# Kernel optimization log

Measured on AMD Instinct MI355X. Metric: run time of the kernel, lower is better.

The kernel has to match this reference:

```python
import jax, jax.numpy as jnp
import numpy as np

TH_HIGH = 0.6
TH_LOW = 0.3
NEGPOS_RATIO = 3
VAR0, VAR1 = 0.1, 0.2
IMG_SIZE = 255.0


def point_form(a):
    # (cx,cy,w,h) -> (xmin,ymin,xmax,ymax)
    return jnp.concatenate([a[..., :2] - a[..., 2:] / 2,
                            a[..., :2] + a[..., 2:] / 2], axis=-1)


def jaccard(a, b):
    # a: [B,4] point form, b: [A,4] point form -> IoU [B,A]
    lt = jnp.maximum(a[:, None, :2], b[None, :, :2])
    rb = jnp.minimum(a[:, None, 2:], b[None, :, 2:])
    wh = jnp.clip(rb - lt, 0.0)
    inter = wh[..., 0] * wh[..., 1]
    area_a = ((a[:, 2] - a[:, 0]) * (a[:, 3] - a[:, 1]))[:, None]
    area_b = ((b[:, 2] - b[:, 0]) * (b[:, 3] - b[:, 1]))[None, :]
    return inter / (area_a + area_b - inter)


def encode(matched, priors):
    # matched: point form, priors: center-size form (standard SSD encode)
    g_cxcy = ((matched[..., :2] + matched[..., 2:]) / 2 - priors[..., :2]) / (VAR0 * priors[..., 2:])
    g_wh = jnp.log((matched[..., 2:] - matched[..., :2]) / priors[..., 2:]) / VAR1
    return jnp.concatenate([g_cxcy, g_wh], axis=-1)


def decode(loc, priors):
    # standard SSD decode -> point form boxes
    cxcy = priors[..., :2] + loc[..., :2] * VAR0 * priors[..., 2:]
    wh = priors[..., 2:] * jnp.exp(loc[..., 2:] * VAR1)
    mins = cxcy - wh / 2
    return jnp.concatenate([mins, mins + wh], axis=-1)


def smooth_l1(x):
    ax = jnp.abs(x)
    return jnp.where(ax < 1.0, 0.5 * x * x, ax - 0.5)


def setup_inputs() -> dict:
    key = jax.random.key(0)
    k1, k2, k3, k4 = jax.random.split(key, 4)
    B, G, S = 64, 128, 4
    A = G * G * S  # 65536 anchors
    c = (jnp.arange(G, dtype=jnp.float32) + 0.5) / G
    cxcy = jnp.stack(jnp.meshgrid(c, c, indexing='ij'), axis=-1).reshape(-1, 2)  # [G*G,2]
    scales = jnp.array([0.08, 0.12, 0.2, 0.3], dtype=jnp.float32)
    wh = jnp.stack([scales, scales], axis=-1)  # [S,2]
    anchors = jnp.concatenate([jnp.repeat(cxcy, S, axis=0), jnp.tile(wh, (G * G, 1))], axis=-1)  # [A,4] center-size
    # gt boxes: small jitter around a random anchor so positives exist
    idx = jax.random.randint(k1, (B,), 0, A)
    gt_cs = anchors[idx] * (1.0 + 0.03 * jax.random.normal(k2, (B, 4), dtype=jnp.float32))
    gt_boxes = point_form(gt_cs)  # [B,4] point form
    loc_pred = 0.5 * jax.random.normal(k3, (B, A, 4), dtype=jnp.float32)
    conf_pred = jax.random.normal(k4, (B, A, 2), dtype=jnp.float32)
    return {"loc_pred": loc_pred, "conf_pred": conf_pred, "gt_boxes": gt_boxes, "anchors": anchors}


def reference(loc_pred, conf_pred, gt_boxes, anchors):
    B, A, _ = loc_pred.shape
    pf_anchors = point_form(anchors)
    overlaps = jaccard(gt_boxes, pf_anchors)                      # [B,A]
    labels = (overlaps >= TH_HIGH).astype(jnp.int32) - \
             ((overlaps > TH_LOW) & (overlaps < TH_HIGH)).astype(jnp.int32)
    pos = labels == 1                                             # [B,A]
    neg0 = labels == 0
    N = pos.sum()
    Nf = jnp.maximum(N.astype(loc_pred.dtype), 1.0)

    loc_gt = encode(gt_boxes[:, None, :], anchors[None, :, :])    # [B,A,4]
    elem = smooth_l1(loc_pred - loc_gt)
    loss_loc = (elem * pos[..., None]).sum() / (Nf * 4.0)

    # --- hard negative mining ---
    logp = jax.nn.log_softmax(conf_pred, axis=-1)                 # [B,A,2]
    tgt = pos.astype(jnp.int32)
    nll = -jnp.take_along_axis(logp, tgt[..., None], axis=-1)[..., 0]  # [B,A]
    ce = jnp.where(neg0, nll, 0.0)
    loss_idx = jnp.argsort(-ce, axis=1)                           # descending
    idx_rank = jnp.argsort(loss_idx, axis=1)
    num_pos = pos.sum(axis=1, keepdims=True)
    num_neg = jnp.clip(NEGPOS_RATIO * num_pos, 10, A - 1)
    neg = idx_rank < num_neg                                      # [B,A]

    # --- weighted classification loss over picked pos+neg ---
    sel = pos | neg
    w = jnp.array([1.0 / 3.0, 1.0], dtype=conf_pred.dtype)
    wsel = jnp.where(sel, w[tgt], 0.0)
    loss_cls = (nll * wsel).sum() / wsel.sum()

    # --- accuracies on picked set ---
    pred_cls = jnp.argmax(conf_pred, axis=-1)
    pos_m = sel & (tgt == 1)
    neg_m = sel & (tgt == 0)
    pos_accuracy = ((pred_cls == 1) & pos_m).sum() / jnp.maximum(pos_m.sum(), 1)
    neg_accuracy = ((pred_cls == 0) & neg_m).sum() / jnp.maximum(neg_m.sum(), 1)

    # --- decoded diagnostics (masked means over positives) ---
    decoded = decode(loc_pred, anchors[None, :, :])               # [B,A,4] point form
    pos_err = jnp.linalg.norm((gt_boxes[:, None, :2] - decoded[..., :2]) * IMG_SIZE, axis=-1)
    position_error = (pos_err * pos).sum() / Nf
    size_diff = jnp.abs(gt_boxes[:, None, 2:] - decoded[..., 2:])  # [B,A,2]
    size_errors = (size_diff * pos[..., None]).sum(axis=(0, 1)) / Nf * IMG_SIZE

    return (loss_loc, loss_cls, pos_accuracy, neg_accuracy, position_error, size_errors, N)
```

## Files before the change

### kernel.cpp

```cpp
#include <hip/hip_runtime.h>
#include <math.h>


#define MAXB 64
#define BPR 16
#define APB 4096
#define KPT 16
#define NB2 4096
#define NB3 2048

struct Accum {
  int pnp[MAXB * BPR];
  int ppc[MAXB * BPR];
  float pf_loc[MAXB * BPR];
  float pf_clsp[MAXB * BPR];
  float pf_perr[MAXB * BPR];
  float pf_se0[MAXB * BPR];
  float pf_se1[MAXB * BPR];
  int cnum[MAXB];
  int b1[MAXB];
  int kr1[MAXB];
  float row_cls[MAXB];
  int row_ntot[MAXB];
  int row_ncor[MAXB];
};

__device__ __forceinline__ float iou_f(float4 g, float4 an) {
  float ax0 = an.x - an.z * 0.5f, ay0 = an.y - an.w * 0.5f;
  float ax1 = an.x + an.z * 0.5f, ay1 = an.y + an.w * 0.5f;
  float ltx = fmaxf(g.x, ax0), lty = fmaxf(g.y, ay0);
  float rbx = fminf(g.z, ax1), rby = fminf(g.w, ay1);
  float w = fmaxf(rbx - ltx, 0.f), h = fmaxf(rby - lty, 0.f);
  float inter = w * h;
  float area_g = (g.z - g.x) * (g.w - g.y);
  float area_a = (ax1 - ax0) * (ay1 - ay0);
  return inter / (area_g + area_a - inter);
}

__device__ __forceinline__ float sl1(float x) {
  float ax = fabsf(x);
  return ax < 1.f ? 0.5f * x * x : ax - 0.5f;
}

__device__ uint2 pick_l1(const unsigned int* __restrict__ g1, int b, int kr_in,
                         unsigned int* s_ws, volatile unsigned int* s_bin,
                         volatile unsigned int* s_kr) {
  int tid = threadIdx.x, lane = tid & 63, wv = tid >> 6;
  const unsigned int* base = g1 + b * BPR * 256;
  unsigned int my = 0;
#pragma unroll
  for (int s = 0; s < BPR; ++s) my += base[s * 256 + tid];
  unsigned int v = my;
#pragma unroll
  for (int o = 1; o < 64; o <<= 1) {
    unsigned int t = __shfl_down(v, o, 64);
    if (lane + o < 64) v += t;
  }
  if (lane == 0) s_ws[wv] = v;
  __syncthreads();
  unsigned int off = 0;
  for (int w2 = wv + 1; w2 < 4; ++w2) off += s_ws[w2];
  unsigned int incl = v + off, above = incl - my;
  if ((int)above < kr_in && kr_in <= (int)incl) {
    *s_bin = (unsigned int)tid;
    *s_kr = (unsigned int)(kr_in - (int)above);
  }
  __syncthreads();
  uint2 r;
  r.x = *s_bin;
  r.y = *s_kr;
  __syncthreads();
  return r;
}

template <int NB>
__device__ uint2 pick_hist(const unsigned int* __restrict__ h, int kr_in,
                           unsigned int* s_ws, volatile unsigned int* s_bin,
                           volatile unsigned int* s_kr) {
  int tid = threadIdx.x, lane = tid & 63, wv = tid >> 6;
  constexpr int PER = NB / 256;
  unsigned int loc[PER];
  unsigned int my = 0;
#pragma unroll
  for (int i = 0; i < PER; ++i) {
    loc[i] = h[tid * PER + i];
    my += loc[i];
  }
  unsigned int v = my;
#pragma unroll
  for (int o = 1; o < 64; o <<= 1) {
    unsigned int t = __shfl_down(v, o, 64);
    if (lane + o < 64) v += t;
  }
  if (lane == 0) s_ws[wv] = v;
  __syncthreads();
  unsigned int off = 0;
  for (int w2 = wv + 1; w2 < 4; ++w2) off += s_ws[w2];
  unsigned int incl = v + off, above = incl - my;
  if ((int)above < kr_in && kr_in <= (int)incl) {
    int kk = kr_in - (int)above;
#pragma unroll
    for (int i = PER - 1; i >= 0; --i) {
      int c = (int)loc[i];
      if (kk <= c) {
        *s_bin = (unsigned int)(tid * PER + i);
        *s_kr = (unsigned int)kk;
        break;
      }
      kk -= c;
    }
  }
  __syncthreads();
  uint2 r;
  r.x = *s_bin;
  r.y = *s_kr;
  __syncthreads();
  return r;
}

__global__ __launch_bounds__(256) void k_main(
    const float* __restrict__ loc_pred, const float* __restrict__ conf,
    const float* __restrict__ gt, const float* __restrict__ anchors,
    Accum* __restrict__ acc, unsigned int* __restrict__ g1,
    unsigned int* __restrict__ g2, int A) {
  int sl = blockIdx.x, b = blockIdx.y;
  int linear = b * BPR + sl;
  int tid = threadIdx.x, lane = tid & 63, wv = tid >> 6;
  __shared__ unsigned int hist[4][256];
  __shared__ float smf[5][4];
  __shared__ int smi[2][4];
  g2[linear * 256 + tid] = 0u;
  if (linear == 0 && tid < MAXB) acc->cnum[tid] = 0;
  for (int i = tid; i < 1024; i += 256) ((unsigned int*)hist)[i] = 0u;
  __syncthreads();

  float4 g4 = reinterpret_cast<const float4*>(gt)[b];
  const float4* conf4 = reinterpret_cast<const float4*>(conf);
  const float4* anc4 = reinterpret_cast<const float4*>(anchors);
  const float4* loc4 = reinterpret_cast<const float4*>(loc_pred);
  int abase = sl * APB;
  long long cbase = ((long long)b * A + abase) >> 1;

  float loc_s = 0.f, clsp = 0.f, perr = 0.f, se0 = 0.f, se1 = 0.f;
  int pcnt = 0, pcor = 0;

#pragma unroll
  for (int j = 0; j < 8; ++j) {
    float4 cc = conf4[cbase + tid + j * 256];
    int a0 = abase + 2 * (tid + j * 256);
#pragma unroll
    for (int h = 0; h < 2; ++h) {
      int a = a0 + h;
      float c0 = h ? cc.z : cc.x;
      float c1 = h ? cc.w : cc.y;
      float4 an = anc4[a];
      float ov = iou_f(g4, an);
      unsigned int kk = 0u;
      if (ov <= 0.3f) {
        float m = fmaxf(c0, c1);
        float s = logf(expf(c0 - m) + expf(c1 - m));
        kk = __float_as_uint((m - c0) + s);
      }
      atomicAdd(&hist[wv][kk >> 23], 1u);
      if (ov >= 0.6f) {
        float4 lp = loc4[(long long)b * A + a];
        float gcx = (g4.x + g4.z) * 0.5f, gcy = (g4.y + g4.w) * 0.5f;
        float gw = g4.z - g4.x, gh = g4.w - g4.y;
        float t0 = (gcx - an.x) / (0.1f * an.z);
        float t1 = (gcy - an.y) / (0.1f * an.w);
        float t2 = logf(gw / an.z) / 0.2f;
        float t3 = logf(gh / an.w) / 0.2f;
        loc_s += sl1(lp.x - t0) + sl1(lp.y - t1) + sl1(lp.z - t2) +
                 sl1(lp.w - t3);
        float m = fmaxf(c0, c1);
        float s = logf(expf(c0 - m) + expf(c1 - m));
        clsp += (m - c1) + s;
        pcnt += 1;
        pcor += (c1 > c0) ? 1 : 0;
        float dcx = an.x + lp.x * 0.1f * an.z;
        float dcy = an.y + lp.y * 0.1f * an.w;
        float dw = an.z * expf(lp.z * 0.2f);
        float dh = an.w * expf(lp.w * 0.2f);
        float dx0 = dcx - dw * 0.5f, dy0 = dcy - dh * 0.5f;
        float ex = (g4.x - dx0) * 255.f, ey = (g4.y - dy0) * 255.f;
        perr += sqrtf(ex * ex + ey * ey);
        se0 += fabsf(g4.z - (dx0 + dw));
        se1 += fabsf(g4.w - (dy0 + dh));
      }
    }
  }

  __syncthreads();
  g1[linear * 256 + tid] =
      hist[0][tid] + hist[1][tid] + hist[2][tid] + hist[3][tid];

  float fv[5] = {loc_s, clsp, perr, se0, se1};
  int iv[2] = {pcnt, pcor};
#pragma unroll
  for (int q = 0; q < 5; ++q) {
    float v = fv[q];
#pragma unroll
    for (int o = 32; o > 0; o >>= 1) v += __shfl_down(v, o, 64);
    if (lane == 0) smf[q][wv] = v;
  }
#pragma unroll
  for (int q = 0; q < 2; ++q) {
    int v = iv[q];
#pragma unroll
    for (int o = 32; o > 0; o >>= 1) v += __shfl_down(v, o, 64);
    if (lane == 0) smi[q][wv] = v;
  }
  __syncthreads();
  if (tid == 0) {
    float L = 0, C = 0, P = 0, S0 = 0, S1 = 0;
    int PC = 0, COR = 0;
    for (int w2 = 0; w2 < 4; ++w2) {
      L += smf[0][w2]; C += smf[1][w2]; P += smf[2][w2];
      S0 += smf[3][w2]; S1 += smf[4][w2];
      PC += smi[0][w2]; COR += smi[1][w2];
    }
    acc->pnp[linear] = PC;
    acc->ppc[linear] = COR;
    acc->pf_loc[linear] = L;
    acc->pf_clsp[linear] = C;
    acc->pf_perr[linear] = P;
    acc->pf_se0[linear] = S0;
    acc->pf_se1[linear] = S1;
  }
}

__global__ __launch_bounds__(256) void k_h2c(
    const float* __restrict__ conf, const float* __restrict__ gt,
    const float* __restrict__ anchors, Accum* __restrict__ acc,
    const unsigned int* __restrict__ g1, unsigned int* __restrict__ g2,
    unsigned int* __restrict__ cbuf, int A) {
  int sl = blockIdx.x, b = blockIdx.y;
  int tid = threadIdx.x, lane = tid & 63, wv = tid >> 6;
  __shared__ unsigned int s_ws[4];
  __shared__ unsigned int s_bin, s_kr;
  __shared__ unsigned int h2[NB2];
  __shared__ unsigned int s_base;

  int np = 0;
#pragma unroll
  for (int s = 0; s < BPR; ++s) np += acc->pnp[b * BPR + s];
  int k = 3 * np;
  if (k < 10) k = 10;
  if (k > A - 1) k = A - 1;
  uint2 p1 = pick_l1(g1, b, k, s_ws, &s_bin, &s_kr);
  unsigned int bin1 = p1.x;
  if (sl == 0 && tid == 0) {
    acc->b1[b] = (int)p1.x;
    acc->kr1[b] = (int)p1.y;
  }
  for (int i = tid; i < NB2; i += 256) h2[i] = 0u;
  __syncthreads();

  float4 g4 = reinterpret_cast<const float4*>(gt)[b];
  const float4* conf4 = reinterpret_cast<const float4*>(conf);
  const float4* anc4 = reinterpret_cast<const float4*>(anchors);
  int abase = sl * APB;
  long long cbase = ((long long)b * A + abase) >> 1;

  unsigned int keys[KPT];
  int cnt = 0;
#pragma unroll
  for (int j = 0; j < 8; ++j) {
    float4 cc = conf4[cbase + tid + j * 256];
    int a0 = abase + 2 * (tid + j * 256);
#pragma unroll
    for (int h = 0; h < 2; ++h) {
      float c0 = h ? cc.z : cc.x;
      float c1 = h ? cc.w : cc.y;
      float4 an = anc4[a0 + h];
      float ov = iou_f(g4, an);
      unsigned int kk = 0u;
      if (ov <= 0.3f) {
        float m = fmaxf(c0, c1);
        float s = logf(expf(c0 - m) + expf(c1 - m));
        kk = __float_as_uint((m - c0) + s);
      }
      if (c1 > c0) kk |= 0x80000000u;
      keys[2 * j + h] = kk;
      unsigned int top8 = (kk & 0x7FFFFFFFu) >> 23;
      if (top8 == bin1) atomicAdd(&h2[(kk >> 11) & 0xFFFu], 1u);
      if (top8 >= bin1) ++cnt;
    }
  }
  __syncthreads();
  for (int i = tid; i < NB2; i += 256)
    if (h2[i]) atomicAdd(&g2[b * NB2 + i], h2[i]);

  unsigned int v = (unsigned int)cnt;
#pragma unroll
  for (int o = 1; o < 64; o <<= 1) {
    unsigned int t = __shfl_up(v, o, 64);
    if (lane >= o) v += t;
  }
  if (lane == 63) s_ws[wv] = v;
  __syncthreads();
  unsigned int woff = 0;
  for (int w2 = 0; w2 < wv; ++w2) woff += s_ws[w2];
  unsigned int excl = woff + v - (unsigned int)cnt;
  if (tid == 0) {
    unsigned int total = s_ws[0] + s_ws[1] + s_ws[2] + s_ws[3];
    s_base = (unsigned int)atomicAdd(&acc->cnum[b], (int)total);
  }
  __syncthreads();
  unsigned int w = s_base + excl;
  unsigned int* crow = cbuf + (size_t)b * A;
#pragma unroll
  for (int j = 0; j < KPT; ++j) {
    unsigned int kk = keys[j];
    if (((kk & 0x7FFFFFFFu) >> 23) >= bin1) crow[w++] = kk;
  }
}

__global__ __launch_bounds__(256) void k_nf(const unsigned int* __restrict__ g2,
                                            const unsigned int* __restrict__ cbuf,
                                            Accum* __restrict__ acc, int A) {
  int b = blockIdx.x;
  int tid = threadIdx.x, lane = tid & 63, wv = tid >> 6;
  __shared__ unsigned int s_ws[4];
  __shared__ unsigned int s_bin, s_kr;
  __shared__ unsigned int h3[NB3];
  __shared__ int s_tie;
  __shared__ float smf[4];
  __shared__ int smi[2][4];

  unsigned int bin1 = (unsigned int)acc->b1[b];
  int kr1 = acc->kr1[b];
  uint2 p2 = pick_hist<NB2>(g2 + b * NB2, kr1, s_ws, &s_bin, &s_kr);
  unsigned int pref20 = (bin1 << 12) | p2.x;
  int cnt = acc->cnum[b];
  for (int i = tid; i < NB3; i += 256) h3[i] = 0u;
  if (tid == 0) s_tie = 0;
  __syncthreads();

  const unsigned int* crow = cbuf + (size_t)b * A;
  for (int i = tid; i < cnt; i += 256) {
    unsigned int k31 = crow[i] & 0x7FFFFFFFu;
    if ((k31 >> 11) == pref20) atomicAdd(&h3[k31 & 0x7FFu], 1u);
  }
  __syncthreads();
  uint2 p3 = pick_hist<NB3>(h3, (int)p2.y, s_ws, &s_bin, &s_kr);
  unsigned int thr = (pref20 << 11) | p3.x;
  int need = (int)p3.y;

  float cls = 0.f;
  int ncnt = 0, ncor = 0;
  for (int i = tid; i < cnt; i += 256) {
    unsigned int kk = crow[i];
    unsigned int k31 = kk & 0x7FFFFFFFu;
    bool s = false;
    if (k31 > thr) {
      s = true;
    } else if (k31 == thr) {
      if (atomicAdd(&s_tie, 1) < need) s = true;
    }
    if (s) {
      cls += __uint_as_float(k31);
      ncnt += 1;
      ncor += (int)((kk >> 31) ^ 1u);
    }
  }
  {
    float v = cls;
#pragma unroll
    for (int o = 32; o > 0; o >>= 1) v += __shfl_down(v, o, 64);
    if (lane == 0) smf[wv] = v;
  }
  {
    int v = ncnt;
#pragma unroll
    for (int o = 32; o > 0; o >>= 1) v += __shfl_down(v, o, 64);
    if (lane == 0) smi[0][wv] = v;
  }
  {
    int v = ncor;
#pragma unroll
    for (int o = 32; o > 0; o >>= 1) v += __shfl_down(v, o, 64);
    if (lane == 0) smi[1][wv] = v;
  }
  __syncthreads();
  if (tid == 0) {
    acc->row_cls[b] = smf[0] + smf[1] + smf[2] + smf[3];
    acc->row_ntot[b] = smi[0][0] + smi[0][1] + smi[0][2] + smi[0][3];
    acc->row_ncor[b] = smi[1][0] + smi[1][1] + smi[1][2] + smi[1][3];
  }
}

__global__ __launch_bounds__(256) void k_final(const Accum* __restrict__ acc,
                                               float* __restrict__ out) {
  __shared__ float sm[256];
  int t = threadIdx.x;
  const int NSL = MAXB * BPR;
  float vals[10];
  float s;
  s = 0; for (int i = t; i < NSL; i += 256) s += acc->pf_loc[i];  vals[0] = s;
  s = 0; for (int i = t; i < NSL; i += 256) s += acc->pf_clsp[i]; vals[1] = s;
  s = 0; for (int i = t; i < NSL; i += 256) s += acc->pf_perr[i]; vals[2] = s;
  s = 0; for (int i = t; i < NSL; i += 256) s += acc->pf_se0[i];  vals[3] = s;
  s = 0; for (int i = t; i < NSL; i += 256) s += acc->pf_se1[i];  vals[4] = s;
  s = 0; for (int i = t; i < MAXB; i += 256) s += acc->row_cls[i]; vals[5] = s;
  s = 0; for (int i = t; i < NSL; i += 256) s += (float)acc->ppc[i]; vals[6] = s;
  s = 0; for (int i = t; i < MAXB; i += 256) s += (float)acc->row_ncor[i]; vals[7] = s;
  s = 0; for (int i = t; i < MAXB; i += 256) s += (float)acc->row_ntot[i]; vals[8] = s;
  s = 0; for (int i = t; i < NSL; i += 256) s += (float)acc->pnp[i]; vals[9] = s;
  float tot[10];
  for (int q = 0; q < 10; ++q) {
    sm[t] = vals[q];
    __syncthreads();
    for (int o = 128; o > 0; o >>= 1) {
      if (t < o) sm[t] += sm[t + o];
      __syncthreads();
    }
    tot[q] = sm[0];
    __syncthreads();
  }
  if (t == 0) {
    float N = tot[9];
    float Nf = fmaxf(N, 1.f);
    out[0] = tot[0] / (Nf * 4.f);
    float wsum = N + tot[8] * (1.f / 3.f);
    out[1] = (tot[1] + tot[5] * (1.f / 3.f)) / wsum;
    out[2] = tot[6] / fmaxf(N, 1.f);
    out[3] = tot[7] / fmaxf(tot[8], 1.f);
    out[4] = tot[2] / Nf;
    out[5] = tot[3] / Nf * 255.f;
    out[6] = tot[4] / Nf * 255.f;
    out[7] = N;
  }
}

extern "C" void kernel_launch(void* const* d_in, const int* in_sizes, int n_in,
                              void* d_out, int out_size, void* d_ws,
                              size_t ws_size, hipStream_t stream) {
  (void)n_in; (void)out_size; (void)ws_size;
  const float* loc = (const float*)d_in[0];
  const float* conf = (const float*)d_in[1];
  const float* gt = (const float*)d_in[2];
  const float* anchors = (const float*)d_in[3];
  int B = in_sizes[2] / 4;
  int A = in_sizes[3] / 4;
  float* out = (float*)d_out;

  char* w = (char*)d_ws;
  Accum* acc = (Accum*)w;
  size_t off = (sizeof(Accum) + 255) & ~(size_t)255;
  unsigned int* g1 = (unsigned int*)(w + off);
  off += (size_t)MAXB * BPR * 256 * 4;
  unsigned int* g2 = (unsigned int*)(w + off);
  off += (size_t)MAXB * NB2 * 4;
  unsigned int* cbuf = (unsigned int*)(w + off);

  dim3 grid(A / APB, B);
  k_main<<<grid, 256, 0, stream>>>(loc, conf, gt, anchors, acc, g1, g2, A);
  k_h2c<<<grid, 256, 0, stream>>>(conf, gt, anchors, acc, g1, g2, cbuf, A);
  k_nf<<<B, 256, 0, stream>>>(g2, cbuf, acc, A);
  k_final<<<1, 256, 0, stream>>>(acc, out);
}
```

Measured before the change: 174.9 us.

## Fuse candidate, threshold and final-reduce kernels with last-block-arrival counters

Merges the compaction, per-row threshold selection and final reduction kernels into a single tail kernel. Each row's last-arriving block, detected through an atomic arrival counter and thread fences, runs the row's second-stage histogram and negative selection. The globally last row block then runs the final reduction. This removes two kernel launches and lets per-row selection start while other rows are still compacting, at the cost of extra fences and atomics and tail work serialized on single blocks.

```diff
diff --git a/kernel.cpp b/kernel.cpp
--- a/kernel.cpp
+++ b/kernel.cpp
@@ -18,8 +18,8 @@
   float pf_se0[MAXB * BPR];
   float pf_se1[MAXB * BPR];
   int cnum[MAXB];
-  int b1[MAXB];
-  int kr1[MAXB];
+  int arrive[MAXB];
+  int done;
   float row_cls[MAXB];
   int row_ntot[MAXB];
   int row_ncor[MAXB];
@@ -130,7 +130,13 @@
   __shared__ float smf[5][4];
   __shared__ int smi[2][4];
   g2[linear * 256 + tid] = 0u;
-  if (linear == 0 && tid < MAXB) acc->cnum[tid] = 0;
+  if (linear == 0) {
+    if (tid < MAXB) {
+      acc->cnum[tid] = 0;
+      acc->arrive[tid] = 0;
+    }
+    if (tid == 0) acc->done = 0;
+  }
   for (int i = tid; i < 1024; i += 256) ((unsigned int*)hist)[i] = 0u;
   __syncthreads();
 
@@ -229,17 +235,22 @@
   }
 }
 
-__global__ __launch_bounds__(256) void k_h2c(
+__global__ __launch_bounds__(256) void k_tail(
     const float* __restrict__ conf, const float* __restrict__ gt,
     const float* __restrict__ anchors, Accum* __restrict__ acc,
     const unsigned int* __restrict__ g1, unsigned int* __restrict__ g2,
-    unsigned int* __restrict__ cbuf, int A) {
+    unsigned int* __restrict__ cbuf, float* __restrict__ out, int A) {
   int sl = blockIdx.x, b = blockIdx.y;
   int tid = threadIdx.x, lane = tid & 63, wv = tid >> 6;
   __shared__ unsigned int s_ws[4];
   __shared__ unsigned int s_bin, s_kr;
-  __shared__ unsigned int h2[NB2];
+  __shared__ unsigned int hbuf[NB2];
   __shared__ unsigned int s_base;
+  __shared__ int s_flag;
+  __shared__ int s_tie;
+  __shared__ float smf[4];
+  __shared__ int smi[2][4];
+  __shared__ float sm[256];
 
   int np = 0;
 #pragma unroll
@@ -249,11 +260,8 @@
   if (k > A - 1) k = A - 1;
   uint2 p1 = pick_l1(g1, b, k, s_ws, &s_bin, &s_kr);
   unsigned int bin1 = p1.x;
-  if (sl == 0 && tid == 0) {
-    acc->b1[b] = (int)p1.x;
-    acc->kr1[b] = (int)p1.y;
-  }
-  for (int i = tid; i < NB2; i += 256) h2[i] = 0u;
+  int kr1 = (int)p1.y;
+  for (int i = tid; i < NB2; i += 256) hbuf[i] = 0u;
   __syncthreads();
 
   float4 g4 = reinterpret_cast<const float4*>(gt)[b];
@@ -283,13 +291,13 @@
       if (c1 > c0) kk |= 0x80000000u;
       keys[2 * j + h] = kk;
       unsigned int top8 = (kk & 0x7FFFFFFFu) >> 23;
-      if (top8 == bin1) atomicAdd(&h2[(kk >> 11) & 0xFFFu], 1u);
+      if (top8 == bin1) atomicAdd(&hbuf[(kk >> 11) & 0xFFFu], 1u);
       if (top8 >= bin1) ++cnt;
     }
   }
   __syncthreads();
   for (int i = tid; i < NB2; i += 256)
-    if (h2[i]) atomicAdd(&g2[b * NB2 + i], h2[i]);
+    if (hbuf[i]) atomicAdd(&g2[b * NB2 + i], hbuf[i]);
 
   unsigned int v = (unsigned int)cnt;
 #pragma unroll
@@ -307,49 +315,42 @@
     s_base = (unsigned int)atomicAdd(&acc->cnum[b], (int)total);
   }
   __syncthreads();
-  unsigned int w = s_base + excl;
+  unsigned int wr = s_base + excl;
   unsigned int* crow = cbuf + (size_t)b * A;
 #pragma unroll
   for (int j = 0; j < KPT; ++j) {
     unsigned int kk = keys[j];
-    if (((kk & 0x7FFFFFFFu) >> 23) >= bin1) crow[w++] = kk;
-  }
-}
-
-__global__ __launch_bounds__(256) void k_nf(const unsigned int* __restrict__ g2,
-                                            const unsigned int* __restrict__ cbuf,
-                                            Accum* __restrict__ acc, int A) {
-  int b = blockIdx.x;
-  int tid = threadIdx.x, lane = tid & 63, wv = tid >> 6;
-  __shared__ unsigned int s_ws[4];
-  __shared__ unsigned int s_bin, s_kr;
-  __shared__ unsigned int h3[NB3];
-  __shared__ int s_tie;
-  __shared__ float smf[4];
-  __shared__ int smi[2][4];
-
-  unsigned int bin1 = (unsigned int)acc->b1[b];
-  int kr1 = acc->kr1[b];
+    if (((kk & 0x7FFFFFFFu) >> 23) >= bin1) crow[wr++] = kk;
+  }
+
+  __threadfence();
+  __syncthreads();
+  if (tid == 0) {
+    int old = atomicAdd(&acc->arrive[b], 1);
+    s_flag = (old == BPR - 1) ? 1 : 0;
+  }
+  __syncthreads();
+  if (!s_flag) return;
+
+  __threadfence();
   uint2 p2 = pick_hist<NB2>(g2 + b * NB2, kr1, s_ws, &s_bin, &s_kr);
   unsigned int pref20 = (bin1 << 12) | p2.x;
-  int cnt = acc->cnum[b];
-  for (int i = tid; i < NB3; i += 256) h3[i] = 0u;
+  int ccnt = acc->cnum[b];
+  for (int i = tid; i < NB3; i += 256) hbuf[i] = 0u;
   if (tid == 0) s_tie = 0;
   __syncthreads();
-
-  const unsigned int* crow = cbuf + (size_t)b * A;
-  for (int i = tid; i < cnt; i += 256) {
+  for (int i = tid; i < ccnt; i += 256) {
     unsigned int k31 = crow[i] & 0x7FFFFFFFu;
-    if ((k31 >> 11) == pref20) atomicAdd(&h3[k31 & 0x7FFu], 1u);
-  }
-  __syncthreads();
-  uint2 p3 = pick_hist<NB3>(h3, (int)p2.y, s_ws, &s_bin, &s_kr);
+    if ((k31 >> 11) == pref20) atomicAdd(&hbuf[k31 & 0x7FFu], 1u);
+  }
+  __syncthreads();
+  uint2 p3 = pick_hist<NB3>(hbuf, (int)p2.y, s_ws, &s_bin, &s_kr);
   unsigned int thr = (pref20 << 11) | p3.x;
   int need = (int)p3.y;
 
   float cls = 0.f;
   int ncnt = 0, ncor = 0;
-  for (int i = tid; i < cnt; i += 256) {
+  for (int i = tid; i < ccnt; i += 256) {
     unsigned int kk = crow[i];
     unsigned int k31 = kk & 0x7FFFFFFFu;
     bool s = false;
@@ -365,22 +366,22 @@
     }
   }
   {
-    float v = cls;
-#pragma unroll
-    for (int o = 32; o > 0; o >>= 1) v += __shfl_down(v, o, 64);
-    if (lane == 0) smf[wv] = v;
+    float vv = cls;
+#pragma unroll
+    for (int o = 32; o > 0; o >>= 1) vv += __shfl_down(vv, o, 64);
+    if (lane == 0) smf[wv] = vv;
   }
   {
-    int v = ncnt;
-#pragma unroll
-    for (int o = 32; o > 0; o >>= 1) v += __shfl_down(v, o, 64);
-    if (lane == 0) smi[0][wv] = v;
+    int vv = ncnt;
+#pragma unroll
+    for (int o = 32; o > 0; o >>= 1) vv += __shfl_down(vv, o, 64);
+    if (lane == 0) smi[0][wv] = vv;
   }
   {
-    int v = ncor;
-#pragma unroll
-    for (int o = 32; o > 0; o >>= 1) v += __shfl_down(v, o, 64);
-    if (lane == 0) smi[1][wv] = v;
+    int vv = ncor;
+#pragma unroll
+    for (int o = 32; o > 0; o >>= 1) vv += __shfl_down(vv, o, 64);
+    if (lane == 0) smi[1][wv] = vv;
   }
   __syncthreads();
   if (tid == 0) {
@@ -388,13 +389,19 @@
     acc->row_ntot[b] = smi[0][0] + smi[0][1] + smi[0][2] + smi[0][3];
     acc->row_ncor[b] = smi[1][0] + smi[1][1] + smi[1][2] + smi[1][3];
   }
-}
-
-__global__ __launch_bounds__(256) void k_final(const Accum* __restrict__ acc,
-                                               float* __restrict__ out) {
-  __shared__ float sm[256];
-  int t = threadIdx.x;
+
+  __threadfence();
+  __syncthreads();
+  if (tid == 0) {
+    int old = atomicAdd(&acc->done, 1);
+    s_flag = (old == MAXB - 1) ? 2 : 0;
+  }
+  __syncthreads();
+  if (s_flag != 2) return;
+  __threadfence();
+
   const int NSL = MAXB * BPR;
+  int t = tid;
   float vals[10];
   float s;
   s = 0; for (int i = t; i < NSL; i += 256) s += acc->pf_loc[i];  vals[0] = s;
@@ -456,7 +463,5 @@
 
   dim3 grid(A / APB, B);
   k_main<<<grid, 256, 0, stream>>>(loc, conf, gt, anchors, acc, g1, g2, A);
-  k_h2c<<<grid, 256, 0, stream>>>(conf, gt, anchors, acc, g1, g2, cbuf, A);
-  k_nf<<<B, 256, 0, stream>>>(g2, cbuf, acc, A);
-  k_final<<<1, 256, 0, stream>>>(acc, out);
-}
+  k_tail<<<grid, 256, 0, stream>>>(conf, gt, anchors, acc, g1, g2, cbuf, out, A);
+}
```

Result: slower. 305.6 us (+74.7%).
